# Kernel tuning notes

Hardware: AMD Instinct MI355X
Metric: run time of the kernel (lower is better)

## Reference

```python
import jax, jax.numpy as jnp
import numpy as np

N = 50000        # nodes
E = 1600000      # edges
R = 20           # relations (num_rels, num_bases == num_rels -> per-relation weights)
IN = 4           # in_dim
H = 64           # hidden_dim
L = 4            # total RGCN layers (num_hidden_layers=3 hidden + 1 output)
EPS = 1e-5       # BatchNorm eps


def setup_inputs() -> dict:
    key = jax.random.key(0)
    ks = jax.random.split(key, 14)
    x = jax.random.normal(ks[0], (N, IN), jnp.float32)
    edge_index = jax.random.randint(ks[1], (2, E), 0, N, jnp.int32)
    edge_type = jax.random.randint(ks[2], (E,), 0, R, jnp.int32)
    # RGCN layer 0: in_dim -> hidden
    W0 = jax.random.normal(ks[3], (R, IN, H), jnp.float32) * 0.1
    root0 = jax.random.normal(ks[4], (IN, H), jnp.float32) * 0.1
    b0 = jax.random.normal(ks[5], (H,), jnp.float32) * 0.1
    # RGCN layers 1..3: hidden -> hidden (stacked)
    Wh = jax.random.normal(ks[6], (L - 1, R, H, H), jnp.float32) * 0.1
    rooth = jax.random.normal(ks[7], (L - 1, H, H), jnp.float32) * 0.1
    bh = jax.random.normal(ks[8], (L - 1, H), jnp.float32) * 0.1
    # BatchNorm (eval mode: running stats) per layer
    gamma = 1.0 + 0.1 * jax.random.normal(ks[9], (L, H), jnp.float32)
    beta = 0.1 * jax.random.normal(ks[10], (L, H), jnp.float32)
    run_mean = 0.1 * jax.random.normal(ks[11], (L, H), jnp.float32)
    run_var = jax.random.uniform(ks[12], (L, H), jnp.float32, 0.5, 1.5)
    return {"x": x, "edge_index": edge_index, "edge_type": edge_type,
            "W0": W0, "root0": root0, "b0": b0,
            "Wh": Wh, "rooth": rooth, "bh": bh,
            "gamma": gamma, "beta": beta,
            "run_mean": run_mean, "run_var": run_var}


def _rgcn(h, src, dst, seg, inv_cnt, W, root, bias):
    # mean-aggregate source features per (relation, dst) segment, then per-relation GEMM
    msum = jax.ops.segment_sum(h[src], seg, num_segments=R * N)  # [R*N, F]
    agg = (msum * inv_cnt).reshape(R, N, -1)                     # [R, N, F]
    return jnp.einsum('rni,rio->no', agg, W) + h @ root + bias   # [N, out]


def _bn_eval(h, g, b, rm, rv):
    return (h - rm) * (g * jax.lax.rsqrt(rv + EPS)) + b


def reference(x, edge_index, edge_type, W0, root0, b0, Wh, rooth, bh,
              gamma, beta, run_mean, run_var):
    src, dst = edge_index[0], edge_index[1]
    seg = edge_type * N + dst  # [E], segment id per (relation, dst)
    cnt = jax.ops.segment_sum(jnp.ones((E,), x.dtype), seg, num_segments=R * N)
    inv_cnt = (1.0 / jnp.maximum(cnt, 1.0))[:, None]  # mean aggregation per relation
    h = x
    for i in range(L):
        W, root, b = (W0, root0, b0) if i == 0 else (Wh[i - 1], rooth[i - 1], bh[i - 1])
        h = _rgcn(h, src, dst, seg, inv_cnt, W, root, b)
        h = _bn_eval(h, gamma[i], beta[i], run_mean[i], run_var[i])
    # last layer (i == num_hidden_layers): relu (dropout is identity in eval)
    return jax.nn.relu(h)
```

## Files before the change

### kernel.cpp

```cpp
#include <hip/hip_runtime.h>

#define NN 50000
#define NE 1600000
#define RR 20
#define BN_EPS 1e-5f
#define SCAN_NB ((NN + 1023) / 1024)

typedef __attribute__((ext_vector_type(8))) short bf16x8;
typedef __attribute__((ext_vector_type(4))) float f32x4;

__device__ __forceinline__ unsigned short f2bf(float f) {
    unsigned u = __float_as_uint(f);
    u += 0x7fff + ((u >> 16) & 1);
    return (unsigned short)(u >> 16);
}
__device__ __forceinline__ void unpack8(uint4 r, float* v) {
    v[0] = __uint_as_float(r.x << 16); v[1] = __uint_as_float(r.x & 0xffff0000u);
    v[2] = __uint_as_float(r.y << 16); v[3] = __uint_as_float(r.y & 0xffff0000u);
    v[4] = __uint_as_float(r.z << 16); v[5] = __uint_as_float(r.z & 0xffff0000u);
    v[6] = __uint_as_float(r.w << 16); v[7] = __uint_as_float(r.w & 0xffff0000u);
}

__global__ void count_kernel(const int* __restrict__ dst, const int* __restrict__ et,
                             int* __restrict__ cnt) {
    int stride = gridDim.x * blockDim.x;
    for (int e = blockIdx.x * blockDim.x + threadIdx.x; e < NE; e += stride)
        atomicAdd(&cnt[dst[e] * RR + et[e]], 1);
}

__global__ void deg_kernel(const int* __restrict__ cnt, int* __restrict__ deg) {
    int stride = gridDim.x * blockDim.x;
    for (int n = blockIdx.x * blockDim.x + threadIdx.x; n < NN; n += stride) {
        int s = 0;
        #pragma unroll
        for (int r = 0; r < RR; ++r) s += cnt[n * RR + r];
        deg[n] = s;
    }
}

__global__ __launch_bounds__(256) void scan1_kernel(const int* __restrict__ in,
                                                    int* __restrict__ out,
                                                    int* __restrict__ bsums, int n) {
    __shared__ int lds[256];
    int tid  = threadIdx.x;
    int base = blockIdx.x * 1024 + tid * 4;
    int v[4];
    #pragma unroll
    for (int j = 0; j < 4; ++j) v[j] = (base + j < n) ? in[base + j] : 0;
    int tsum = v[0] + v[1] + v[2] + v[3];
    lds[tid] = tsum;
    __syncthreads();
    for (int off = 1; off < 256; off <<= 1) {
        int t = (tid >= off) ? lds[tid - off] : 0;
        __syncthreads();
        lds[tid] += t;
        __syncthreads();
    }
    int run = lds[tid] - tsum;
    #pragma unroll
    for (int j = 0; j < 4; ++j) {
        if (base + j < n) out[base + j] = run;
        run += v[j];
    }
    if (tid == 255) bsums[blockIdx.x] = lds[255];
}

__global__ __launch_bounds__(1024) void scan_top_kernel(int* __restrict__ bsums, int nb) {
    __shared__ int lds[1024];
    int tid = threadIdx.x;
    int v = (tid < nb) ? bsums[tid] : 0;
    lds[tid] = v;
    __syncthreads();
    for (int off = 1; off < 1024; off <<= 1) {
        int t = (tid >= off) ? lds[tid - off] : 0;
        __syncthreads();
        lds[tid] += t;
        __syncthreads();
    }
    bsums[tid] = lds[tid] - v;
}

__global__ void scan_add_kernel(int* __restrict__ out, const int* __restrict__ bsums, int n) {
    int stride = gridDim.x * blockDim.x;
    int i = blockIdx.x * blockDim.x + threadIdx.x;
    if (i == 0) out[NN] = NE;
    for (; i < n; i += stride)
        out[i] += bsums[i >> 10];
}

__global__ void fill_kernel(const int* __restrict__ src, const int* __restrict__ dst,
                            const int* __restrict__ et, const int* __restrict__ offs,
                            const int* __restrict__ cntdr,
                            int* __restrict__ fill, uint2* __restrict__ ep) {
    int stride = gridDim.x * blockDim.x;
    for (int e = blockIdx.x * blockDim.x + threadIdx.x; e < NE; e += stride) {
        int d = dst[e], r = et[e];
        int pos = offs[d] + atomicAdd(&fill[d], 1);
        int c = cntdr[d * RR + r];
        float ic = 1.0f / (float)(c > 0 ? c : 1);
        ep[pos] = make_uint2((unsigned)src[e] | ((unsigned)r << 20),
                             __float_as_uint(ic));
    }
}

__global__ __launch_bounds__(256) void wprep_kernel(const float* __restrict__ Wh,
                                                    const float* __restrict__ rooth,
                                                    unsigned short* __restrict__ Wt) {
    int l = blockIdx.x / 21, r = blockIdx.x % 21;
    const float* Ws = (r < 20) ? Wh + ((size_t)l * 20 + r) * 4096
                               : rooth + (size_t)l * 4096;
    unsigned short* Wd = Wt + ((size_t)l * 21 + r) * 4096;
    int t = threadIdx.x;
    int n4 = (t & 15) * 4;
    for (int k = t >> 4; k < 64; k += 16) {
        float4 w = *(const float4*)&Ws[(size_t)k * 64 + n4];
        Wd[(n4 + 0) * 64 + k] = f2bf(w.x);
        Wd[(n4 + 1) * 64 + k] = f2bf(w.y);
        Wd[(n4 + 2) * 64 + k] = f2bf(w.z);
        Wd[(n4 + 3) * 64 + k] = f2bf(w.w);
    }
}

__global__ __launch_bounds__(256) void agg0_kernel(
    const float* __restrict__ x, const int* __restrict__ offs,
    const uint2* __restrict__ ep,
    const float* __restrict__ W0, const float* __restrict__ root0,
    const float* __restrict__ b0, const float* __restrict__ gamma,
    const float* __restrict__ beta, const float* __restrict__ rmean,
    const float* __restrict__ rvar, unsigned short* __restrict__ outb) {
    __shared__ float Wl[21 * 256];
    int tid = threadIdx.x;
    for (int i = tid; i < 21 * 256; i += 256)
        Wl[i] = (i < 20 * 256) ? W0[i] : root0[i - 20 * 256];
    __syncthreads();

    int wid   = (blockIdx.x * 256 + tid) >> 6;
    int nw    = (gridDim.x * 256) >> 6;
    int lane  = tid & 63;
    int eslot = lane >> 3;
    int flane = lane & 7;

    for (int n = wid; n < NN; n += nw) {
        int e0 = offs[n], e1 = offs[n + 1];
        float a[8] = {0, 0, 0, 0, 0, 0, 0, 0};
        for (int e = e0 + eslot; e < e1; e += 8) {
            uint2 m = ep[e];
            float ic = __uint_as_float(m.y);
            float4 xv = *(const float4*)&x[(size_t)(m.x & 0xFFFFF) * 4];
            const float* w = &Wl[(m.x >> 20) * 256 + flane * 8];
            float4 w0 = *(const float4*)&w[0],   w0b = *(const float4*)&w[4];
            float4 w1 = *(const float4*)&w[64],  w1b = *(const float4*)&w[68];
            float4 w2 = *(const float4*)&w[128], w2b = *(const float4*)&w[132];
            float4 w3 = *(const float4*)&w[192], w3b = *(const float4*)&w[196];
            a[0] += ic * (xv.x * w0.x + xv.y * w1.x + xv.z * w2.x + xv.w * w3.x);
            a[1] += ic * (xv.x * w0.y + xv.y * w1.y + xv.z * w2.y + xv.w * w3.y);
            a[2] += ic * (xv.x * w0.z + xv.y * w1.z + xv.z * w2.z + xv.w * w3.z);
            a[3] += ic * (xv.x * w0.w + xv.y * w1.w + xv.z * w2.w + xv.w * w3.w);
            a[4] += ic * (xv.x * w0b.x + xv.y * w1b.x + xv.z * w2b.x + xv.w * w3b.x);
            a[5] += ic * (xv.x * w0b.y + xv.y * w1b.y + xv.z * w2b.y + xv.w * w3b.y);
            a[6] += ic * (xv.x * w0b.z + xv.y * w1b.z + xv.z * w2b.z + xv.w * w3b.z);
            a[7] += ic * (xv.x * w0b.w + xv.y * w1b.w + xv.z * w2b.w + xv.w * w3b.w);
        }
        #pragma unroll
        for (int off = 8; off < 64; off <<= 1)
            #pragma unroll
            for (int j = 0; j < 8; ++j) a[j] += __shfl_xor(a[j], off);

        if (eslot == 0) {
            float4 xn = *(const float4*)&x[(size_t)n * 4];
            const float* w = &Wl[20 * 256 + flane * 8];
            float v[8];
            #pragma unroll
            for (int j = 0; j < 8; ++j) {
                a[j] += xn.x * w[j] + xn.y * w[64 + j] + xn.z * w[128 + j] + xn.w * w[192 + j];
                int col = flane * 8 + j;
                float s = gamma[col] * rsqrtf(rvar[col] + BN_EPS);
                v[j] = (a[j] + b0[col] - rmean[col]) * s + beta[col];
            }
            ushort4 p0, p1;
            p0.x = f2bf(v[0]); p0.y = f2bf(v[1]); p0.z = f2bf(v[2]); p0.w = f2bf(v[3]);
            p1.x = f2bf(v[4]); p1.y = f2bf(v[5]); p1.z = f2bf(v[6]); p1.w = f2bf(v[7]);
            *(ushort4*)&outb[(size_t)n * 64 + flane * 8]     = p0;
            *(ushort4*)&outb[(size_t)n * 64 + flane * 8 + 4] = p1;
        }
    }
}

__global__ __launch_bounds__(256) void xform_kernel(
    const unsigned short* __restrict__ hin, const unsigned short* __restrict__ WtL,
    unsigned short* __restrict__ T, int c0) {
    __shared__ unsigned short tile[64 * 72];
    const int tid  = threadIdx.x;
    const int n0   = blockIdx.x * 64;
    const int r    = blockIdx.y;
    const int wv   = tid >> 6;
    const int lane = tid & 63;
    const int frow = lane & 15;
    const int kgrp = lane >> 4;
    int arc = min(n0 + wv * 16 + frow, NN - 1);
    bf16x8 a0 = *(const bf16x8*)&hin[(size_t)arc * 64 + kgrp * 8];
    bf16x8 a1 = *(const bf16x8*)&hin[(size_t)arc * 64 + 32 + kgrp * 8];
    const unsigned short* Wr = WtL + (size_t)(c0 + r) * 4096;
    unsigned short* Tr = T + (size_t)r * NN * 64;
    #pragma unroll
    for (int cf = 0; cf < 4; ++cf) {
        bf16x8 b0 = *(const bf16x8*)&Wr[(cf * 16 + frow) * 64 + kgrp * 8];
        bf16x8 b1 = *(const bf16x8*)&Wr[(cf * 16 + frow) * 64 + 32 + kgrp * 8];
        f32x4 d = {0.f, 0.f, 0.f, 0.f};
        d = __builtin_amdgcn_mfma_f32_16x16x32_bf16(a0, b0, d, 0, 0, 0);
        d = __builtin_amdgcn_mfma_f32_16x16x32_bf16(a1, b1, d, 0, 0, 0);
        #pragma unroll
        for (int j = 0; j < 4; ++j)
            tile[(wv * 16 + kgrp * 4 + j) * 72 + cf * 16 + frow] = f2bf(d[j]);
    }
    __syncthreads();
    #pragma unroll
    for (int i = tid; i < 512; i += 256) {
        int row = i >> 3, c16 = i & 7;
        int node = n0 + row;
        if (node < NN)
            *(uint4*)&Tr[(size_t)node * 64 + c16 * 8] =
                *(const uint4*)&tile[row * 72 + c16 * 8];
    }
}

template <bool FIRST, bool LASTP, bool LASTL>
__global__ __launch_bounds__(256) void agg_kernel(
    const unsigned short* __restrict__ T, const int* __restrict__ offs,
    const uint2* __restrict__ ep, float* __restrict__ accum, int c0, int c1,
    const float* __restrict__ bias, const float* __restrict__ gamma,
    const float* __restrict__ beta, const float* __restrict__ rmean,
    const float* __restrict__ rvar, unsigned short* __restrict__ outb,
    float* __restrict__ outf) {
    constexpr bool FULL = FIRST && LASTP;
    int wid   = (blockIdx.x * 256 + threadIdx.x) >> 6;
    int nw    = (gridDim.x * 256) >> 6;
    int lane  = threadIdx.x & 63;
    int eslot = lane >> 3;
    int flane = lane & 7;
    const unsigned ce = (c1 < RR) ? (unsigned)c1 : (unsigned)RR;

    for (int n = wid; n < NN; n += nw) {
        int e0 = offs[n], e1 = offs[n + 1];
        float a[8] = {0, 0, 0, 0, 0, 0, 0, 0};
        for (int e = e0 + eslot; e < e1; e += 8) {
            uint2 m = ep[e];
            unsigned r = m.x >> 20;
            if (FULL || (r >= (unsigned)c0 && r < ce)) {
                float ic = __uint_as_float(m.y);
                size_t ti = ((size_t)(r - c0) * NN + (m.x & 0xFFFFF)) * 64;
                uint4 row = *(const uint4*)&T[ti + flane * 8];
                float v[8]; unpack8(row, v);
                #pragma unroll
                for (int j = 0; j < 8; ++j) a[j] += ic * v[j];
            }
        }
        #pragma unroll
        for (int off = 8; off < 64; off <<= 1)
            #pragma unroll
            for (int j = 0; j < 8; ++j) a[j] += __shfl_xor(a[j], off);

        if (eslot == 0) {
            if (LASTP) {
                uint4 rr = *(const uint4*)&T[((size_t)(20 - c0) * NN + n) * 64 + flane * 8];
                float rv[8]; unpack8(rr, rv);
                #pragma unroll
                for (int j = 0; j < 8; ++j) a[j] += rv[j];
            }
            if (!FIRST) {
                float4 p0 = *(const float4*)&accum[(size_t)n * 64 + flane * 8];
                float4 p1 = *(const float4*)&accum[(size_t)n * 64 + flane * 8 + 4];
                a[0] += p0.x; a[1] += p0.y; a[2] += p0.z; a[3] += p0.w;
                a[4] += p1.x; a[5] += p1.y; a[6] += p1.z; a[7] += p1.w;
            }
            if (!LASTP) {
                *(float4*)&accum[(size_t)n * 64 + flane * 8] =
                    make_float4(a[0], a[1], a[2], a[3]);
                *(float4*)&accum[(size_t)n * 64 + flane * 8 + 4] =
                    make_float4(a[4], a[5], a[6], a[7]);
            } else {
                float v[8];
                #pragma unroll
                for (int j = 0; j < 8; ++j) {
                    int col = flane * 8 + j;
                    float s = gamma[col] * rsqrtf(rvar[col] + BN_EPS);
                    v[j] = (a[j] + bias[col] - rmean[col]) * s + beta[col];
                }
                if (LASTL) {
                    float4 o0 = make_float4(fmaxf(v[0],0.f), fmaxf(v[1],0.f),
                                            fmaxf(v[2],0.f), fmaxf(v[3],0.f));
                    float4 o1 = make_float4(fmaxf(v[4],0.f), fmaxf(v[5],0.f),
                                            fmaxf(v[6],0.f), fmaxf(v[7],0.f));
                    *(float4*)&outf[(size_t)n * 64 + flane * 8]     = o0;
                    *(float4*)&outf[(size_t)n * 64 + flane * 8 + 4] = o1;
                } else {
                    ushort4 p0, p1;
                    p0.x = f2bf(v[0]); p0.y = f2bf(v[1]);
                    p0.z = f2bf(v[2]); p0.w = f2bf(v[3]);
                    p1.x = f2bf(v[4]); p1.y = f2bf(v[5]);
                    p1.z = f2bf(v[6]); p1.w = f2bf(v[7]);
                    *(ushort4*)&outb[(size_t)n * 64 + flane * 8]     = p0;
                    *(ushort4*)&outb[(size_t)n * 64 + flane * 8 + 4] = p1;
                }
            }
        }
    }
}

extern "C" void kernel_launch(void* const* d_in, const int* in_sizes, int n_in,
                              void* d_out, int out_size, void* d_ws, size_t ws_size,
                              hipStream_t stream) {
    const float* x     = (const float*)d_in[0];
    const int*   ei    = (const int*)d_in[1];
    const int*   et    = (const int*)d_in[2];
    const float* W0    = (const float*)d_in[3];
    const float* root0 = (const float*)d_in[4];
    const float* b0    = (const float*)d_in[5];
    const float* Wh    = (const float*)d_in[6];
    const float* rooth = (const float*)d_in[7];
    const float* bh    = (const float*)d_in[8];
    const float* gamma = (const float*)d_in[9];
    const float* beta  = (const float*)d_in[10];
    const float* rmean = (const float*)d_in[11];
    const float* rvar  = (const float*)d_in[12];
    float* out = (float*)d_out;

    const int* src = ei;
    const int* dst = ei + NE;

    int*   cntdr = (int*)d_ws;
    int*   deg   = cntdr + 1000000;
    int*   fill  = deg + 50000;
    int*   offs  = fill + 50000;
    int*   bsums = offs + 50004;
    uint2* ep    = (uint2*)(bsums + 1024);
    unsigned short* Wt = (unsigned short*)(ep + NE);
    unsigned short* h0 = Wt + 3 * 21 * 4096;
    unsigned short* h1 = h0 + NN * 64;
    float* accum = (float*)(h1 + NN * 64);
    unsigned short* T = (unsigned short*)(accum + NN * 64);

    size_t used  = (size_t)((char*)T - (char*)d_ws);
    size_t avail = (ws_size > used) ? ws_size - used : 0;
    size_t per   = (size_t)NN * 64 * 2;
    int nrel = (int)(avail / per);
    if (nrel < 1) nrel = 1;
    if (nrel > 21) nrel = 21;
    int npass = (21 + nrel - 1) / nrel;

    hipMemsetAsync(cntdr, 0, (size_t)NN * RR * sizeof(int), stream);
    hipMemsetAsync(fill, 0, (size_t)NN * sizeof(int), stream);
    count_kernel<<<2048, 256, 0, stream>>>(dst, et, cntdr);
    deg_kernel<<<256, 256, 0, stream>>>(cntdr, deg);
    scan1_kernel<<<SCAN_NB, 256, 0, stream>>>(deg, offs, bsums, NN);
    scan_top_kernel<<<1, 1024, 0, stream>>>(bsums, SCAN_NB);
    scan_add_kernel<<<256, 256, 0, stream>>>(offs, bsums, NN);
    fill_kernel<<<2048, 256, 0, stream>>>(src, dst, et, offs, cntdr, fill, ep);
    wprep_kernel<<<63, 256, 0, stream>>>(Wh, rooth, Wt);

    agg0_kernel<<<2048, 256, 0, stream>>>(
        x, offs, ep, W0, root0, b0, gamma, beta, rmean, rvar, h0);

    const int XB = (NN + 63) / 64;
    for (int l = 1; l < 4; ++l) {
        const unsigned short* hin = (l == 2) ? h1 : h0;
        unsigned short* hout = (l == 1) ? h1 : h0;
        const float* bl  = bh + (size_t)(l - 1) * 64;
        const float* gl  = gamma + (size_t)l * 64;
        const float* btl = beta + (size_t)l * 64;
        const float* rml = rmean + (size_t)l * 64;
        const float* rvl = rvar + (size_t)l * 64;
        int c0 = 0;
        for (int p = 0; p < npass; ++p) {
            int c1 = c0 + nrel; if (c1 > 21) c1 = 21;
            dim3 xg(XB, c1 - c0);
            xform_kernel<<<xg, 256, 0, stream>>>(
                hin, Wt + (size_t)(l - 1) * 21 * 4096, T, c0);
            bool first = (p == 0), lastp = (p == npass - 1);
            bool lastl = lastp && (l == 3);
            #define AGG(F, LP, LL) agg_kernel<F, LP, LL><<<2048, 256, 0, stream>>>( \
                T, offs, ep, accum, c0, c1, bl, gl, btl, rml, rvl, hout, out)
            if (first && lastp && lastl)      AGG(true,  true,  true);
            else if (first && lastp)          AGG(true,  true,  false);
            else if (first)                   AGG(true,  false, false);
            else if (lastp && lastl)          AGG(false, true,  true);
            else if (lastp)                   AGG(false, true,  false);
            else                              AGG(false, false, false);
            #undef AGG
            c0 = c1;
        }
    }
}
```

Baseline: 734.5 us.

## Aggregate-then-transform: per-node relation sums followed by one wide GEMM

Changes each hidden layer from transforming features per relation (T = h·W_r for all 21 relations, then gathering from T) to first gathering raw 64-wide source features into per-relation sums in shared memory with LDS atomics. These sums are written as a [N, 21·64] bf16 matrix together with the root features, then multiplied by a concatenated weight matrix in one MFMA GEMM with fused bias, BatchNorm and ReLU. This removes the large per-relation T buffer writes, the multi-pass scheme and the fp32 accumulate buffer. In exchange it adds LDS atomic contention, a 134 MB msum buffer write and read per layer, and an extra bf16 rounding of the aggregated sums.

```diff
diff --git a/kernel.cpp b/kernel.cpp
--- a/kernel.cpp
+++ b/kernel.cpp
@@ -4,6 +4,7 @@
 #define NE 1600000
 #define RR 20
 #define BN_EPS 1e-5f
+#define KK (21 * 64)
 #define SCAN_NB ((NN + 1023) / 1024)
 
 typedef __attribute__((ext_vector_type(8))) short bf16x8;
@@ -105,19 +106,19 @@
 
 __global__ __launch_bounds__(256) void wprep_kernel(const float* __restrict__ Wh,
                                                     const float* __restrict__ rooth,
-                                                    unsigned short* __restrict__ Wt) {
+                                                    unsigned short* __restrict__ Wg) {
     int l = blockIdx.x / 21, r = blockIdx.x % 21;
     const float* Ws = (r < 20) ? Wh + ((size_t)l * 20 + r) * 4096
                                : rooth + (size_t)l * 4096;
-    unsigned short* Wd = Wt + ((size_t)l * 21 + r) * 4096;
+    unsigned short* Wd = Wg + (size_t)l * 64 * KK + r * 64;
     int t = threadIdx.x;
     int n4 = (t & 15) * 4;
     for (int k = t >> 4; k < 64; k += 16) {
         float4 w = *(const float4*)&Ws[(size_t)k * 64 + n4];
-        Wd[(n4 + 0) * 64 + k] = f2bf(w.x);
-        Wd[(n4 + 1) * 64 + k] = f2bf(w.y);
-        Wd[(n4 + 2) * 64 + k] = f2bf(w.z);
-        Wd[(n4 + 3) * 64 + k] = f2bf(w.w);
+        Wd[(size_t)(n4 + 0) * KK + k] = f2bf(w.x);
+        Wd[(size_t)(n4 + 1) * KK + k] = f2bf(w.y);
+        Wd[(size_t)(n4 + 2) * KK + k] = f2bf(w.z);
+        Wd[(size_t)(n4 + 3) * KK + k] = f2bf(w.w);
     }
 }
 
@@ -186,123 +187,135 @@
     }
 }
 
-__global__ __launch_bounds__(256) void xform_kernel(
-    const unsigned short* __restrict__ hin, const unsigned short* __restrict__ WtL,
-    unsigned short* __restrict__ T, int c0) {
-    __shared__ unsigned short tile[64 * 72];
+__global__ __launch_bounds__(256) void msum_kernel(
+    const unsigned short* __restrict__ hin, const int* __restrict__ offs,
+    const uint2* __restrict__ ep, unsigned short* __restrict__ msum) {
+    constexpr int RP = 68;
+    __shared__ float acc[4][20 * RP];
+    const int tid   = threadIdx.x;
+    const int wv    = tid >> 6;
+    const int lane  = tid & 63;
+    const int wid   = (blockIdx.x * 256 + tid) >> 6;
+    const int nw    = (gridDim.x * 256) >> 6;
+    const int eslot = lane >> 3;
+    const int flane = lane & 7;
+    float* A = acc[wv];
+
+    for (int n = wid; n < NN; n += nw) {
+        float4 z4 = make_float4(0.f, 0.f, 0.f, 0.f);
+        #pragma unroll
+        for (int i = 0; i < 6; ++i) {
+            int idx = i * 64 + lane;
+            if (idx < 340) ((float4*)A)[idx] = z4;
+        }
+        int e0 = offs[n], e1 = offs[n + 1];
+        for (int e = e0 + eslot; e < e1; e += 8) {
+            uint2 m = ep[e];
+            float ic = __uint_as_float(m.y);
+            int s = m.x & 0xFFFFF;
+            int r = m.x >> 20;
+            uint4 row = *(const uint4*)&hin[(size_t)s * 64 + flane * 8];
+            float v[8]; unpack8(row, v);
+            float* p = &A[r * RP + flane * 8];
+            #pragma unroll
+            for (int j = 0; j < 8; ++j) atomicAdd(p + j, ic * v[j]);
+        }
+        unsigned* out = (unsigned*)&msum[(size_t)n * KK];
+        #pragma unroll
+        for (int i = 0; i < 10; ++i) {
+            int idx = i * 64 + lane;
+            int idx2 = idx * 2;
+            int r = idx2 >> 6, f = idx2 & 63;
+            float lo = A[r * RP + f], hi = A[r * RP + f + 1];
+            out[idx] = (unsigned)f2bf(lo) | ((unsigned)f2bf(hi) << 16);
+        }
+        if (lane < 32)
+            out[640 + lane] = ((const unsigned*)&hin[(size_t)n * 64])[lane];
+    }
+}
+
+template <bool LAST>
+__global__ __launch_bounds__(256) void gemm_kernel(
+    const unsigned short* __restrict__ msum, const unsigned short* __restrict__ Wg,
+    const float* __restrict__ bias, const float* __restrict__ gamma,
+    const float* __restrict__ beta, const float* __restrict__ rmean,
+    const float* __restrict__ rvar, unsigned short* __restrict__ outb,
+    float* __restrict__ outf) {
+    __shared__ unsigned short stage[2][64 * 72];
+    unsigned short* Al = stage[0];
+    unsigned short* Bl = stage[1];
     const int tid  = threadIdx.x;
-    const int n0   = blockIdx.x * 64;
-    const int r    = blockIdx.y;
     const int wv   = tid >> 6;
     const int lane = tid & 63;
     const int frow = lane & 15;
     const int kgrp = lane >> 4;
-    int arc = min(n0 + wv * 16 + frow, NN - 1);
-    bf16x8 a0 = *(const bf16x8*)&hin[(size_t)arc * 64 + kgrp * 8];
-    bf16x8 a1 = *(const bf16x8*)&hin[(size_t)arc * 64 + 32 + kgrp * 8];
-    const unsigned short* Wr = WtL + (size_t)(c0 + r) * 4096;
-    unsigned short* Tr = T + (size_t)r * NN * 64;
+    const int n0   = blockIdx.x * 64;
+
+    f32x4 acc[4];
     #pragma unroll
-    for (int cf = 0; cf < 4; ++cf) {
-        bf16x8 b0 = *(const bf16x8*)&Wr[(cf * 16 + frow) * 64 + kgrp * 8];
-        bf16x8 b1 = *(const bf16x8*)&Wr[(cf * 16 + frow) * 64 + 32 + kgrp * 8];
-        f32x4 d = {0.f, 0.f, 0.f, 0.f};
-        d = __builtin_amdgcn_mfma_f32_16x16x32_bf16(a0, b0, d, 0, 0, 0);
-        d = __builtin_amdgcn_mfma_f32_16x16x32_bf16(a1, b1, d, 0, 0, 0);
-        #pragma unroll
-        for (int j = 0; j < 4; ++j)
-            tile[(wv * 16 + kgrp * 4 + j) * 72 + cf * 16 + frow] = f2bf(d[j]);
-    }
+    for (int cb = 0; cb < 4; ++cb) acc[cb] = (f32x4){0.f, 0.f, 0.f, 0.f};
+
+    const int srow = tid >> 3;
+    const int sch  = tid & 7;
+    const int gnA0 = min(n0 + srow, NN - 1);
+    const int gnA1 = min(n0 + srow + 32, NN - 1);
+
+    for (int k0 = 0; k0 < KK; k0 += 64) {
+        __syncthreads();
+        *(uint4*)&Al[srow * 72 + sch * 8] =
+            *(const uint4*)&msum[(size_t)gnA0 * KK + k0 + sch * 8];
+        *(uint4*)&Al[(srow + 32) * 72 + sch * 8] =
+            *(const uint4*)&msum[(size_t)gnA1 * KK + k0 + sch * 8];
+        *(uint4*)&Bl[srow * 72 + sch * 8] =
+            *(const uint4*)&Wg[(size_t)srow * KK + k0 + sch * 8];
+        *(uint4*)&Bl[(srow + 32) * 72 + sch * 8] =
+            *(const uint4*)&Wg[(size_t)(srow + 32) * KK + k0 + sch * 8];
+        __syncthreads();
+        #pragma unroll
+        for (int ks = 0; ks < 2; ++ks) {
+            bf16x8 a = *(bf16x8*)&Al[(wv * 16 + frow) * 72 + ks * 32 + kgrp * 8];
+            #pragma unroll
+            for (int cb = 0; cb < 4; ++cb) {
+                bf16x8 b = *(bf16x8*)&Bl[(cb * 16 + frow) * 72 + ks * 32 + kgrp * 8];
+                acc[cb] = __builtin_amdgcn_mfma_f32_16x16x32_bf16(a, b, acc[cb], 0, 0, 0);
+            }
+        }
+    }
+
     __syncthreads();
     #pragma unroll
-    for (int i = tid; i < 512; i += 256) {
-        int row = i >> 3, c16 = i & 7;
-        int node = n0 + row;
-        if (node < NN)
-            *(uint4*)&Tr[(size_t)node * 64 + c16 * 8] =
-                *(const uint4*)&tile[row * 72 + c16 * 8];
-    }
-}
-
-template <bool FIRST, bool LASTP, bool LASTL>
-__global__ __launch_bounds__(256) void agg_kernel(
-    const unsigned short* __restrict__ T, const int* __restrict__ offs,
-    const uint2* __restrict__ ep, float* __restrict__ accum, int c0, int c1,
-    const float* __restrict__ bias, const float* __restrict__ gamma,
-    const float* __restrict__ beta, const float* __restrict__ rmean,
-    const float* __restrict__ rvar, unsigned short* __restrict__ outb,
-    float* __restrict__ outf) {
-    constexpr bool FULL = FIRST && LASTP;
-    int wid   = (blockIdx.x * 256 + threadIdx.x) >> 6;
-    int nw    = (gridDim.x * 256) >> 6;
-    int lane  = threadIdx.x & 63;
-    int eslot = lane >> 3;
-    int flane = lane & 7;
-    const unsigned ce = (c1 < RR) ? (unsigned)c1 : (unsigned)RR;
-
-    for (int n = wid; n < NN; n += nw) {
-        int e0 = offs[n], e1 = offs[n + 1];
-        float a[8] = {0, 0, 0, 0, 0, 0, 0, 0};
-        for (int e = e0 + eslot; e < e1; e += 8) {
-            uint2 m = ep[e];
-            unsigned r = m.x >> 20;
-            if (FULL || (r >= (unsigned)c0 && r < ce)) {
-                float ic = __uint_as_float(m.y);
-                size_t ti = ((size_t)(r - c0) * NN + (m.x & 0xFFFFF)) * 64;
-                uint4 row = *(const uint4*)&T[ti + flane * 8];
-                float v[8]; unpack8(row, v);
-                #pragma unroll
-                for (int j = 0; j < 8; ++j) a[j] += ic * v[j];
-            }
-        }
-        #pragma unroll
-        for (int off = 8; off < 64; off <<= 1)
-            #pragma unroll
-            for (int j = 0; j < 8; ++j) a[j] += __shfl_xor(a[j], off);
-
-        if (eslot == 0) {
-            if (LASTP) {
-                uint4 rr = *(const uint4*)&T[((size_t)(20 - c0) * NN + n) * 64 + flane * 8];
-                float rv[8]; unpack8(rr, rv);
-                #pragma unroll
-                for (int j = 0; j < 8; ++j) a[j] += rv[j];
-            }
-            if (!FIRST) {
-                float4 p0 = *(const float4*)&accum[(size_t)n * 64 + flane * 8];
-                float4 p1 = *(const float4*)&accum[(size_t)n * 64 + flane * 8 + 4];
-                a[0] += p0.x; a[1] += p0.y; a[2] += p0.z; a[3] += p0.w;
-                a[4] += p1.x; a[5] += p1.y; a[6] += p1.z; a[7] += p1.w;
-            }
-            if (!LASTP) {
-                *(float4*)&accum[(size_t)n * 64 + flane * 8] =
-                    make_float4(a[0], a[1], a[2], a[3]);
-                *(float4*)&accum[(size_t)n * 64 + flane * 8 + 4] =
-                    make_float4(a[4], a[5], a[6], a[7]);
-            } else {
-                float v[8];
-                #pragma unroll
-                for (int j = 0; j < 8; ++j) {
-                    int col = flane * 8 + j;
-                    float s = gamma[col] * rsqrtf(rvar[col] + BN_EPS);
-                    v[j] = (a[j] + bias[col] - rmean[col]) * s + beta[col];
-                }
-                if (LASTL) {
-                    float4 o0 = make_float4(fmaxf(v[0],0.f), fmaxf(v[1],0.f),
-                                            fmaxf(v[2],0.f), fmaxf(v[3],0.f));
-                    float4 o1 = make_float4(fmaxf(v[4],0.f), fmaxf(v[5],0.f),
-                                            fmaxf(v[6],0.f), fmaxf(v[7],0.f));
-                    *(float4*)&outf[(size_t)n * 64 + flane * 8]     = o0;
-                    *(float4*)&outf[(size_t)n * 64 + flane * 8 + 4] = o1;
-                } else {
-                    ushort4 p0, p1;
-                    p0.x = f2bf(v[0]); p0.y = f2bf(v[1]);
-                    p0.z = f2bf(v[2]); p0.w = f2bf(v[3]);
-                    p1.x = f2bf(v[4]); p1.y = f2bf(v[5]);
-                    p1.z = f2bf(v[6]); p1.w = f2bf(v[7]);
-                    *(ushort4*)&outb[(size_t)n * 64 + flane * 8]     = p0;
-                    *(ushort4*)&outb[(size_t)n * 64 + flane * 8 + 4] = p1;
-                }
-            }
+    for (int cb = 0; cb < 4; ++cb) {
+        int col = cb * 16 + frow;
+        float s  = gamma[col] * rsqrtf(rvar[col] + BN_EPS);
+        float sh = beta[col] - rmean[col] * s;
+        float bi = bias[col];
+        #pragma unroll
+        for (int j = 0; j < 4; ++j) {
+            float v = (acc[cb][j] + bi) * s + sh;
+            int row = wv * 16 + kgrp * 4 + j;
+            if (LAST) ((float*)stage)[row * 72 + col] = fmaxf(v, 0.f);
+            else      Al[row * 72 + col] = f2bf(v);
+        }
+    }
+    __syncthreads();
+    if (LAST) {
+        const float* F = (const float*)stage;
+        #pragma unroll
+        for (int i = tid; i < 1024; i += 256) {
+            int row = i >> 4, c4 = i & 15;
+            int node = n0 + row;
+            if (node < NN)
+                *(float4*)&outf[(size_t)node * 64 + c4 * 4] =
+                    *(const float4*)&F[row * 72 + c4 * 4];
+        }
+    } else {
+        #pragma unroll
+        for (int i = tid; i < 512; i += 256) {
+            int row = i >> 3, c8 = i & 7;
+            int node = n0 + row;
+            if (node < NN)
+                *(uint4*)&outb[(size_t)node * 64 + c8 * 8] =
+                    *(const uint4*)&Al[row * 72 + c8 * 8];
         }
     }
 }
@@ -334,19 +347,10 @@
     int*   offs  = fill + 50000;
     int*   bsums = offs + 50004;
     uint2* ep    = (uint2*)(bsums + 1024);
-    unsigned short* Wt = (unsigned short*)(ep + NE);
-    unsigned short* h0 = Wt + 3 * 21 * 4096;
+    unsigned short* Wg = (unsigned short*)(ep + NE);
+    unsigned short* h0 = Wg + 3 * 64 * KK;
     unsigned short* h1 = h0 + NN * 64;
-    float* accum = (float*)(h1 + NN * 64);
-    unsigned short* T = (unsigned short*)(accum + NN * 64);
-
-    size_t used  = (size_t)((char*)T - (char*)d_ws);
-    size_t avail = (ws_size > used) ? ws_size - used : 0;
-    size_t per   = (size_t)NN * 64 * 2;
-    int nrel = (int)(avail / per);
-    if (nrel < 1) nrel = 1;
-    if (nrel > 21) nrel = 21;
-    int npass = (21 + nrel - 1) / nrel;
+    unsigned short* msum = h1 + NN * 64;
 
     hipMemsetAsync(cntdr, 0, (size_t)NN * RR * sizeof(int), stream);
     hipMemsetAsync(fill, 0, (size_t)NN * sizeof(int), stream);
@@ -356,12 +360,12 @@
     scan_top_kernel<<<1, 1024, 0, stream>>>(bsums, SCAN_NB);
     scan_add_kernel<<<256, 256, 0, stream>>>(offs, bsums, NN);
     fill_kernel<<<2048, 256, 0, stream>>>(src, dst, et, offs, cntdr, fill, ep);
-    wprep_kernel<<<63, 256, 0, stream>>>(Wh, rooth, Wt);
+    wprep_kernel<<<63, 256, 0, stream>>>(Wh, rooth, Wg);
 
     agg0_kernel<<<2048, 256, 0, stream>>>(
         x, offs, ep, W0, root0, b0, gamma, beta, rmean, rvar, h0);
 
-    const int XB = (NN + 63) / 64;
+    const int GB = (NN + 63) / 64;
     for (int l = 1; l < 4; ++l) {
         const unsigned short* hin = (l == 2) ? h1 : h0;
         unsigned short* hout = (l == 1) ? h1 : h0;
@@ -370,24 +374,13 @@
         const float* btl = beta + (size_t)l * 64;
         const float* rml = rmean + (size_t)l * 64;
         const float* rvl = rvar + (size_t)l * 64;
-        int c0 = 0;
-        for (int p = 0; p < npass; ++p) {
-            int c1 = c0 + nrel; if (c1 > 21) c1 = 21;
-            dim3 xg(XB, c1 - c0);
-            xform_kernel<<<xg, 256, 0, stream>>>(
-                hin, Wt + (size_t)(l - 1) * 21 * 4096, T, c0);
-            bool first = (p == 0), lastp = (p == npass - 1);
-            bool lastl = lastp && (l == 3);
-            #define AGG(F, LP, LL) agg_kernel<F, LP, LL><<<2048, 256, 0, stream>>>( \
-                T, offs, ep, accum, c0, c1, bl, gl, btl, rml, rvl, hout, out)
-            if (first && lastp && lastl)      AGG(true,  true,  true);
-            else if (first && lastp)          AGG(true,  true,  false);
-            else if (first)                   AGG(true,  false, false);
-            else if (lastp && lastl)          AGG(false, true,  true);
-            else if (lastp)                   AGG(false, true,  false);
-            else                              AGG(false, false, false);
-            #undef AGG
-            c0 = c1;
-        }
-    }
-}
+        const unsigned short* WgL = Wg + (size_t)(l - 1) * 64 * KK;
+        msum_kernel<<<2048, 256, 0, stream>>>(hin, offs, ep, msum);
+        if (l == 3)
+            gemm_kernel<true><<<GB, 256, 0, stream>>>(
+                msum, WgL, bl, gl, btl, rml, rvl, nullptr, out);
+        else
+            gemm_kernel<false><<<GB, 256, 0, stream>>>(
+                msum, WgL, bl, gl, btl, rml, rvl, hout, nullptr);
+    }
+}
```

Result: slower. 2.025 ms (+175.7%).

## Compute per-relation mean counts on the fly and tile xform over relations

Applied to the files above, without the earlier changes.

Drops the dense per-(node, relation) count array, its memset and its count kernel. Edge records shrink from 8 to 4 bytes, and each aggregation wave rebuilds per-relation inverse counts for its node with LDS atomics in an extra pass over the node's edges. The xform kernel now processes 128 nodes and up to 3 relations per block, reusing the loaded A fragments across relations. The cost is a second edge-list scan in every aggregation kernel, and the cross-lane LDS reads rely on intra-wave ordering without an explicit barrier.

```diff
diff --git a/kernel.cpp b/kernel.cpp
--- a/kernel.cpp
+++ b/kernel.cpp
@@ -21,21 +21,10 @@
     v[6] = __uint_as_float(r.w << 16); v[7] = __uint_as_float(r.w & 0xffff0000u);
 }
 
-__global__ void count_kernel(const int* __restrict__ dst, const int* __restrict__ et,
-                             int* __restrict__ cnt) {
+__global__ void deg_kernel(const int* __restrict__ dst, int* __restrict__ deg) {
     int stride = gridDim.x * blockDim.x;
     for (int e = blockIdx.x * blockDim.x + threadIdx.x; e < NE; e += stride)
-        atomicAdd(&cnt[dst[e] * RR + et[e]], 1);
-}
-
-__global__ void deg_kernel(const int* __restrict__ cnt, int* __restrict__ deg) {
-    int stride = gridDim.x * blockDim.x;
-    for (int n = blockIdx.x * blockDim.x + threadIdx.x; n < NN; n += stride) {
-        int s = 0;
-        #pragma unroll
-        for (int r = 0; r < RR; ++r) s += cnt[n * RR + r];
-        deg[n] = s;
-    }
+        atomicAdd(&deg[dst[e]], 1);
 }
 
 __global__ __launch_bounds__(256) void scan1_kernel(const int* __restrict__ in,
@@ -90,16 +79,12 @@
 
 __global__ void fill_kernel(const int* __restrict__ src, const int* __restrict__ dst,
                             const int* __restrict__ et, const int* __restrict__ offs,
-                            const int* __restrict__ cntdr,
-                            int* __restrict__ fill, uint2* __restrict__ ep) {
+                            int* __restrict__ fill, unsigned* __restrict__ ep) {
     int stride = gridDim.x * blockDim.x;
     for (int e = blockIdx.x * blockDim.x + threadIdx.x; e < NE; e += stride) {
-        int d = dst[e], r = et[e];
+        int d = dst[e];
         int pos = offs[d] + atomicAdd(&fill[d], 1);
-        int c = cntdr[d * RR + r];
-        float ic = 1.0f / (float)(c > 0 ? c : 1);
-        ep[pos] = make_uint2((unsigned)src[e] | ((unsigned)r << 20),
-                             __float_as_uint(ic));
+        ep[pos] = (unsigned)src[e] | ((unsigned)et[e] << 20);
     }
 }
 
@@ -123,12 +108,14 @@
 
 __global__ __launch_bounds__(256) void agg0_kernel(
     const float* __restrict__ x, const int* __restrict__ offs,
-    const uint2* __restrict__ ep,
+    const unsigned* __restrict__ ep,
     const float* __restrict__ W0, const float* __restrict__ root0,
     const float* __restrict__ b0, const float* __restrict__ gamma,
     const float* __restrict__ beta, const float* __restrict__ rmean,
     const float* __restrict__ rvar, unsigned short* __restrict__ outb) {
     __shared__ float Wl[21 * 256];
+    __shared__ int   cw[4][24];
+    __shared__ float fw[4][24];
     int tid = threadIdx.x;
     for (int i = tid; i < 21 * 256; i += 256)
         Wl[i] = (i < 20 * 256) ? W0[i] : root0[i - 20 * 256];
@@ -136,18 +123,28 @@
 
     int wid   = (blockIdx.x * 256 + tid) >> 6;
     int nw    = (gridDim.x * 256) >> 6;
+    int wv    = tid >> 6;
     int lane  = tid & 63;
     int eslot = lane >> 3;
     int flane = lane & 7;
 
     for (int n = wid; n < NN; n += nw) {
         int e0 = offs[n], e1 = offs[n + 1];
+        if (lane < 20) cw[wv][lane] = 0;
+        for (int e = e0 + eslot; e < e1; e += 8) {
+            unsigned m = ep[e];
+            if (flane == 0) atomicAdd(&cw[wv][m >> 20], 1);
+        }
+        if (lane < 20) {
+            int c = cw[wv][lane];
+            fw[wv][lane] = 1.0f / (float)(c > 0 ? c : 1);
+        }
         float a[8] = {0, 0, 0, 0, 0, 0, 0, 0};
         for (int e = e0 + eslot; e < e1; e += 8) {
-            uint2 m = ep[e];
-            float ic = __uint_as_float(m.y);
-            float4 xv = *(const float4*)&x[(size_t)(m.x & 0xFFFFF) * 4];
-            const float* w = &Wl[(m.x >> 20) * 256 + flane * 8];
+            unsigned m = ep[e];
+            float ic = fw[wv][m >> 20];
+            float4 xv = *(const float4*)&x[(size_t)(m & 0xFFFFF) * 4];
+            const float* w = &Wl[(m >> 20) * 256 + flane * 8];
             float4 w0 = *(const float4*)&w[0],   w0b = *(const float4*)&w[4];
             float4 w1 = *(const float4*)&w[64],  w1b = *(const float4*)&w[68];
             float4 w2 = *(const float4*)&w[128], w2b = *(const float4*)&w[132];
@@ -188,67 +185,93 @@
 
 __global__ __launch_bounds__(256) void xform_kernel(
     const unsigned short* __restrict__ hin, const unsigned short* __restrict__ WtL,
-    unsigned short* __restrict__ T, int c0) {
-    __shared__ unsigned short tile[64 * 72];
+    unsigned short* __restrict__ T, int c0, int nr) {
+    __shared__ unsigned short tile[128 * 72];
     const int tid  = threadIdx.x;
-    const int n0   = blockIdx.x * 64;
-    const int r    = blockIdx.y;
+    const int n0   = blockIdx.x * 128;
+    const int rg   = blockIdx.y;
     const int wv   = tid >> 6;
     const int lane = tid & 63;
     const int frow = lane & 15;
     const int kgrp = lane >> 4;
-    int arc = min(n0 + wv * 16 + frow, NN - 1);
-    bf16x8 a0 = *(const bf16x8*)&hin[(size_t)arc * 64 + kgrp * 8];
-    bf16x8 a1 = *(const bf16x8*)&hin[(size_t)arc * 64 + 32 + kgrp * 8];
-    const unsigned short* Wr = WtL + (size_t)(c0 + r) * 4096;
-    unsigned short* Tr = T + (size_t)r * NN * 64;
+
+    bf16x8 a[2][2];
     #pragma unroll
-    for (int cf = 0; cf < 4; ++cf) {
-        bf16x8 b0 = *(const bf16x8*)&Wr[(cf * 16 + frow) * 64 + kgrp * 8];
-        bf16x8 b1 = *(const bf16x8*)&Wr[(cf * 16 + frow) * 64 + 32 + kgrp * 8];
-        f32x4 d = {0.f, 0.f, 0.f, 0.f};
-        d = __builtin_amdgcn_mfma_f32_16x16x32_bf16(a0, b0, d, 0, 0, 0);
-        d = __builtin_amdgcn_mfma_f32_16x16x32_bf16(a1, b1, d, 0, 0, 0);
+    for (int g = 0; g < 2; ++g) {
+        int arc = min(n0 + wv * 32 + g * 16 + frow, NN - 1);
+        a[g][0] = *(const bf16x8*)&hin[(size_t)arc * 64 + kgrp * 8];
+        a[g][1] = *(const bf16x8*)&hin[(size_t)arc * 64 + 32 + kgrp * 8];
+    }
+
+    int rend = min(rg * 3 + 3, nr);
+    for (int r = rg * 3; r < rend; ++r) {
+        const unsigned short* Wr = WtL + (size_t)(c0 + r) * 4096;
+        unsigned short* Tr = T + (size_t)r * NN * 64;
         #pragma unroll
-        for (int j = 0; j < 4; ++j)
-            tile[(wv * 16 + kgrp * 4 + j) * 72 + cf * 16 + frow] = f2bf(d[j]);
-    }
-    __syncthreads();
-    #pragma unroll
-    for (int i = tid; i < 512; i += 256) {
-        int row = i >> 3, c16 = i & 7;
-        int node = n0 + row;
-        if (node < NN)
-            *(uint4*)&Tr[(size_t)node * 64 + c16 * 8] =
-                *(const uint4*)&tile[row * 72 + c16 * 8];
+        for (int cb = 0; cb < 4; ++cb) {
+            bf16x8 b0 = *(const bf16x8*)&Wr[(cb * 16 + frow) * 64 + kgrp * 8];
+            bf16x8 b1 = *(const bf16x8*)&Wr[(cb * 16 + frow) * 64 + 32 + kgrp * 8];
+            #pragma unroll
+            for (int g = 0; g < 2; ++g) {
+                f32x4 d = {0.f, 0.f, 0.f, 0.f};
+                d = __builtin_amdgcn_mfma_f32_16x16x32_bf16(a[g][0], b0, d, 0, 0, 0);
+                d = __builtin_amdgcn_mfma_f32_16x16x32_bf16(a[g][1], b1, d, 0, 0, 0);
+                #pragma unroll
+                for (int j = 0; j < 4; ++j)
+                    tile[(wv * 32 + g * 16 + kgrp * 4 + j) * 72 + cb * 16 + frow] = f2bf(d[j]);
+            }
+        }
+        __syncthreads();
+        #pragma unroll
+        for (int i = tid; i < 1024; i += 256) {
+            int row = i >> 3, c8 = i & 7;
+            int node = n0 + row;
+            if (node < NN)
+                *(uint4*)&Tr[(size_t)node * 64 + c8 * 8] =
+                    *(const uint4*)&tile[row * 72 + c8 * 8];
+        }
+        __syncthreads();
     }
 }
 
 template <bool FIRST, bool LASTP, bool LASTL>
 __global__ __launch_bounds__(256) void agg_kernel(
     const unsigned short* __restrict__ T, const int* __restrict__ offs,
-    const uint2* __restrict__ ep, float* __restrict__ accum, int c0, int c1,
+    const unsigned* __restrict__ ep, float* __restrict__ accum, int c0, int c1,
     const float* __restrict__ bias, const float* __restrict__ gamma,
     const float* __restrict__ beta, const float* __restrict__ rmean,
     const float* __restrict__ rvar, unsigned short* __restrict__ outb,
     float* __restrict__ outf) {
     constexpr bool FULL = FIRST && LASTP;
+    __shared__ int   cw[4][24];
+    __shared__ float fw[4][24];
     int wid   = (blockIdx.x * 256 + threadIdx.x) >> 6;
     int nw    = (gridDim.x * 256) >> 6;
+    int wv    = threadIdx.x >> 6;
     int lane  = threadIdx.x & 63;
     int eslot = lane >> 3;
     int flane = lane & 7;
-    const unsigned ce = (c1 < RR) ? (unsigned)c1 : (unsigned)RR;
+    const unsigned uc0 = (unsigned)c0;
+    const unsigned ce  = (c1 < RR) ? (unsigned)c1 : (unsigned)RR;
 
     for (int n = wid; n < NN; n += nw) {
         int e0 = offs[n], e1 = offs[n + 1];
+        if (lane < 20) cw[wv][lane] = 0;
+        for (int e = e0 + eslot; e < e1; e += 8) {
+            unsigned m = ep[e];
+            if (flane == 0) atomicAdd(&cw[wv][m >> 20], 1);
+        }
+        if (lane < 20) {
+            int c = cw[wv][lane];
+            fw[wv][lane] = 1.0f / (float)(c > 0 ? c : 1);
+        }
         float a[8] = {0, 0, 0, 0, 0, 0, 0, 0};
         for (int e = e0 + eslot; e < e1; e += 8) {
-            uint2 m = ep[e];
-            unsigned r = m.x >> 20;
-            if (FULL || (r >= (unsigned)c0 && r < ce)) {
-                float ic = __uint_as_float(m.y);
-                size_t ti = ((size_t)(r - c0) * NN + (m.x & 0xFFFFF)) * 64;
+            unsigned m = ep[e];
+            unsigned r = m >> 20;
+            if (FULL || (r >= uc0 && r < ce)) {
+                float ic = fw[wv][r];
+                size_t ti = ((size_t)(r - uc0) * NN + (m & 0xFFFFF)) * 64;
                 uint4 row = *(const uint4*)&T[ti + flane * 8];
                 float v[8]; unpack8(row, v);
                 #pragma unroll
@@ -262,7 +285,7 @@
 
         if (eslot == 0) {
             if (LASTP) {
-                uint4 rr = *(const uint4*)&T[((size_t)(20 - c0) * NN + n) * 64 + flane * 8];
+                uint4 rr = *(const uint4*)&T[((size_t)(20 - uc0) * NN + n) * 64 + flane * 8];
                 float rv[8]; unpack8(rr, rv);
                 #pragma unroll
                 for (int j = 0; j < 8; ++j) a[j] += rv[j];
@@ -328,12 +351,11 @@
     const int* src = ei;
     const int* dst = ei + NE;
 
-    int*   cntdr = (int*)d_ws;
-    int*   deg   = cntdr + 1000000;
-    int*   fill  = deg + 50000;
-    int*   offs  = fill + 50000;
-    int*   bsums = offs + 50004;
-    uint2* ep    = (uint2*)(bsums + 1024);
+    int*      deg   = (int*)d_ws;
+    int*      fill  = deg + 50000;
+    int*      offs  = fill + 50000;
+    int*      bsums = offs + 50004;
+    unsigned* ep    = (unsigned*)(bsums + 1024);
     unsigned short* Wt = (unsigned short*)(ep + NE);
     unsigned short* h0 = Wt + 3 * 21 * 4096;
     unsigned short* h1 = h0 + NN * 64;
@@ -348,20 +370,19 @@
     if (nrel > 21) nrel = 21;
     int npass = (21 + nrel - 1) / nrel;
 
-    hipMemsetAsync(cntdr, 0, (size_t)NN * RR * sizeof(int), stream);
+    hipMemsetAsync(deg, 0, (size_t)NN * sizeof(int), stream);
     hipMemsetAsync(fill, 0, (size_t)NN * sizeof(int), stream);
-    count_kernel<<<2048, 256, 0, stream>>>(dst, et, cntdr);
-    deg_kernel<<<256, 256, 0, stream>>>(cntdr, deg);
+    deg_kernel<<<2048, 256, 0, stream>>>(dst, deg);
     scan1_kernel<<<SCAN_NB, 256, 0, stream>>>(deg, offs, bsums, NN);
     scan_top_kernel<<<1, 1024, 0, stream>>>(bsums, SCAN_NB);
     scan_add_kernel<<<256, 256, 0, stream>>>(offs, bsums, NN);
-    fill_kernel<<<2048, 256, 0, stream>>>(src, dst, et, offs, cntdr, fill, ep);
+    fill_kernel<<<2048, 256, 0, stream>>>(src, dst, et, offs, fill, ep);
     wprep_kernel<<<63, 256, 0, stream>>>(Wh, rooth, Wt);
 
     agg0_kernel<<<2048, 256, 0, stream>>>(
         x, offs, ep, W0, root0, b0, gamma, beta, rmean, rvar, h0);
 
-    const int XB = (NN + 63) / 64;
+    const int XB = (NN + 127) / 128;
     for (int l = 1; l < 4; ++l) {
         const unsigned short* hin = (l == 2) ? h1 : h0;
         unsigned short* hout = (l == 1) ? h1 : h0;
@@ -373,9 +394,10 @@
         int c0 = 0;
         for (int p = 0; p < npass; ++p) {
             int c1 = c0 + nrel; if (c1 > 21) c1 = 21;
-            dim3 xg(XB, c1 - c0);
+            int nr = c1 - c0;
+            dim3 xg(XB, (nr + 2) / 3);
             xform_kernel<<<xg, 256, 0, stream>>>(
-                hin, Wt + (size_t)(l - 1) * 21 * 4096, T, c0);
+                hin, Wt + (size_t)(l - 1) * 21 * 4096, T, c0, nr);
             bool first = (p == 0), lastp = (p == npass - 1);
             bool lastl = lastp && (l == 3);
             #define AGG(F, LP, LL) agg_kernel<F, LP, LL><<<2048, 256, 0, stream>>>( \
```

Result: no change. 726.0 us (-1.2%).
